# Performance work log

Hardware: AMD Instinct MI355X
Metric: run time of the kernel (lower is better)

The kernel has to match this reference:

```python
import jax, jax.numpy as jnp
import numpy as np

B, S, NX = 2, 2048, 1024
N_STATE, N_HEAD = 1024, 16
HEAD_DIM = N_STATE // N_HEAD


def setup_inputs() -> dict:
    key = jax.random.key(0)
    k1, k2, k3 = jax.random.split(key, 3)
    x = jax.random.normal(k1, (B, S, NX), dtype=jnp.float32)
    w_c = jax.random.normal(k2, (NX, 3 * N_STATE), dtype=jnp.float32) * 0.02
    b_c = jnp.zeros((3 * N_STATE,), dtype=jnp.float32)
    w_p = jax.random.normal(k3, (NX, N_STATE), dtype=jnp.float32) * 0.02
    b_p = jnp.zeros((N_STATE,), dtype=jnp.float32)
    return {"x": x, "w_c": w_c, "b_c": b_c, "w_p": w_p, "b_p": b_p}


def reference(x, w_c, b_c, w_p, b_p):
    # c_attn: 1x1 conv == dense over last dim -> [B, S, 3*n_state]
    c = jnp.einsum('bsn,nf->bsf', x, w_c) + b_c
    q, k, v = jnp.split(c, 3, axis=2)

    def split_heads(t):  # [B,S,n_state] -> [B,H,S,D]
        return t.reshape(B, S, N_HEAD, HEAD_DIM).transpose(0, 2, 1, 3)

    q = split_heads(q)
    k = split_heads(k)  # we contract over D directly instead of transposing to [B,H,D,S]
    v = split_heads(v)

    # scores [B,H,S,S], scaled by rsqrt(head_dim) (scale=True)
    w = jnp.einsum('bhqd,bhkd->bhqk', q, k) * jax.lax.rsqrt(jnp.float32(HEAD_DIM))
    # band mask exactly as in source: w*b + -1e9*(1-b)
    band = jnp.tril(jnp.ones((S, S), dtype=jnp.float32))[None, None]
    w = w * band + (-1e9) * (1.0 - band)
    w = jax.nn.softmax(w, axis=-1)
    a = jnp.einsum('bhqk,bhkd->bhqd', w, v)

    # merge heads -> [B,S,n_state]
    a = a.transpose(0, 2, 1, 3).reshape(B, S, N_STATE)
    # c_proj
    out = jnp.einsum('bsn,nf->bsf', a, w_p) + b_p
    return out
```

## Files before the change

### kernel.cpp

```cpp
#include <hip/hip_runtime.h>
#include <math.h>

#define BATCH 2
#define SEQ 2048
#define NX 1024
#define NSTATE 1024
#define NHEAD 16
#define HDIM 64
#define QKV_LD (3*NSTATE)

typedef __attribute__((ext_vector_type(4))) float f32x4;
typedef __attribute__((ext_vector_type(8))) short bf16x8;

__device__ __forceinline__ unsigned short f2bf(float x) {
    unsigned int u = __float_as_uint(x);
    u = (u + 0x7FFFu + ((u >> 16) & 1u)) >> 16;
    return (unsigned short)u;
}

__device__ __forceinline__ unsigned int cvtpk_bf16(float a, float b) {
    unsigned int r;
    asm("v_cvt_pk_bf16_f32 %0, %1, %2" : "=v"(r) : "v"(a), "v"(b));
    return r;
}

#define GLL(src, dst) __builtin_amdgcn_global_load_lds( \
    (const __attribute__((address_space(1))) void*)(src), \
    (__attribute__((address_space(3))) void*)(dst), 16, 0, 0)

__global__ __launch_bounds__(256) void prep_kernel(
    const float* __restrict__ x, const float* __restrict__ w_c,
    const float* __restrict__ w_p,
    unsigned short* __restrict__ xbf, unsigned short* __restrict__ wcT,
    unsigned short* __restrict__ wpT)
{
    const int bx = blockIdx.x;
    const int t = threadIdx.x;
    if (bx < 4096) {
        int i = bx * 256 + t;
        float4 v = ((const float4*)x)[i];
        ushort4 o;
        o.x = f2bf(v.x); o.y = f2bf(v.y); o.z = f2bf(v.z); o.w = f2bf(v.w);
        ((ushort4*)xbf)[i] = o;
        return;
    }
    __shared__ float tile[64][65];
    const float* in;
    unsigned short* out;
    int R, C, c0, r0;
    if (bx < 4096 + 768) {
        int idx = bx - 4096;
        in = w_c; out = wcT; R = NX; C = 3 * NSTATE;
        c0 = (idx % 48) * 64; r0 = (idx / 48) * 64;
    } else {
        int idx = bx - 4864;
        in = w_p; out = wpT; R = NX; C = NSTATE;
        c0 = (idx % 16) * 64; r0 = (idx / 16) * 64;
    }
    const int cc = t & 63;
    const int rb = t >> 6;
    #pragma unroll
    for (int i = 0; i < 16; i++) {
        int rr = rb + i * 4;
        tile[rr][cc] = in[(size_t)(r0 + rr) * C + c0 + cc];
    }
    __syncthreads();
    #pragma unroll
    for (int i = 0; i < 16; i++) {
        int rr = rb + i * 4;
        out[(size_t)(c0 + rr) * R + r0 + cc] = f2bf(tile[cc][rr]);
    }
}

__global__ __launch_bounds__(256) void vtrans_kernel(
    const unsigned short* __restrict__ qkv, unsigned short* __restrict__ vt)
{
    __shared__ unsigned short t[64][72];
    const int s0 = blockIdx.x * 64;
    const int bh = blockIdx.y;
    const int b = bh >> 4, h = bh & 15;
    const int r = threadIdx.x >> 2;
    const int cg = (threadIdx.x & 3) * 16;
    const unsigned short* src = qkv + (size_t)(b * SEQ + s0 + r) * QKV_LD
                                + 2 * NSTATE + h * HDIM + cg;
    *(bf16x8*)&t[r][cg]     = *(const bf16x8*)src;
    *(bf16x8*)&t[r][cg + 8] = *(const bf16x8*)(src + 8);
    __syncthreads();
    unsigned short tmp[16];
    #pragma unroll
    for (int i = 0; i < 16; i++) tmp[i] = t[cg + i][r];
    unsigned short* dst = vt + (size_t)(bh * 64 + r) * SEQ + s0 + cg;
    *(bf16x8*)dst       = ((const bf16x8*)tmp)[0];
    *(bf16x8*)(dst + 8) = ((const bf16x8*)tmp)[1];
}

template<int RX, int RY, int NBX, bool BF16_OUT>
__global__ __launch_bounds__(256) void gemm_bf16(
    const unsigned short* __restrict__ A,
    const unsigned short* __restrict__ BT,
    const float* __restrict__ bias,
    void* __restrict__ Cv, int M, int N, int K)
{
    const int flat = blockIdx.x;
    const int xcd = flat & 7;
    const int j = flat >> 3;
    const int bx = (xcd % (NBX / RX)) * RX + (j % RX);
    const int by = (xcd / (NBX / RX)) * RY + (j / RX);

    __shared__ unsigned short Als[128 * 32];
    __shared__ unsigned short Bls[128 * 32];
    const int tid = threadIdx.x;
    const int wave = tid >> 6, lane = tid & 63;
    const int bm = bx * 128, bn = by * 128;
    const int wr = (wave >> 1) * 64, wc = (wave & 1) * 64;

    f32x4 acc[4][4];
    #pragma unroll
    for (int m = 0; m < 4; m++)
        #pragma unroll
        for (int n = 0; n < 4; n++)
            acc[m][n] = (f32x4){0.f, 0.f, 0.f, 0.f};

    const int arow = tid >> 2;
    const int ac8 = (tid & 3) * 8;
    char* alds0 = (char*)Als + wave * 1024;
    char* blds0 = (char*)Bls + wave * 1024;
    const int fr = lane & 15, kq = (lane >> 4) * 8;

    for (int k0 = 0; k0 < K; k0 += 32) {
        const unsigned short* ga0 = A  + (size_t)(bm + arow) * K + k0 + ac8;
        const unsigned short* gb0 = BT + (size_t)(bn + arow) * K + k0 + ac8;
        GLL(ga0, alds0);
        GLL(ga0 + (size_t)64 * K, alds0 + 4096);
        GLL(gb0, blds0);
        GLL(gb0 + (size_t)64 * K, blds0 + 4096);
        __syncthreads();

        bf16x8 af[4], bfr[4];
        #pragma unroll
        for (int m = 0; m < 4; m++)
            af[m] = *(const bf16x8*)&Als[(wr + m * 16 + fr) * 32 + kq];
        #pragma unroll
        for (int n = 0; n < 4; n++)
            bfr[n] = *(const bf16x8*)&Bls[(wc + n * 16 + fr) * 32 + kq];
        #pragma unroll
        for (int m = 0; m < 4; m++)
            #pragma unroll
            for (int n = 0; n < 4; n++)
                acc[m][n] = __builtin_amdgcn_mfma_f32_16x16x32_bf16(
                    af[m], bfr[n], acc[m][n], 0, 0, 0);
        __syncthreads();
    }

    const int cr = (lane >> 4) * 4;
    const int ccol = lane & 15;
    #pragma unroll
    for (int m = 0; m < 4; m++) {
        const int row = bm + wr + m * 16 + cr;
        #pragma unroll
        for (int n = 0; n < 4; n++) {
            const int col = bn + wc + n * 16 + ccol;
            const float bv = bias[col];
            #pragma unroll
            for (int j2 = 0; j2 < 4; j2++) {
                float v = acc[m][n][j2] + bv;
                if (BF16_OUT)
                    ((unsigned short*)Cv)[(size_t)(row + j2) * N + col] = f2bf(v);
                else
                    ((float*)Cv)[(size_t)(row + j2) * N + col] = v;
            }
        }
    }
}

template<int RX, int RY, int NBX, bool BF16_OUT>
__global__ __launch_bounds__(256) void gemm_bf16_s(
    const unsigned short* __restrict__ A,
    const unsigned short* __restrict__ BT,
    const float* __restrict__ bias,
    void* __restrict__ Cv, int M, int N, int K)
{
    const int flat = blockIdx.x;
    const int xcd = flat & 7;
    const int j = flat >> 3;
    const int bx = (xcd % (NBX / RX)) * RX + (j % RX);
    const int by = (xcd / (NBX / RX)) * RY + (j / RX);

    __shared__ unsigned short Als[64 * 32];
    __shared__ unsigned short Bls[64 * 32];
    const int tid = threadIdx.x;
    const int wave = tid >> 6, lane = tid & 63;
    const int bm = bx * 64, bn = by * 64;
    const int wr = (wave >> 1) * 32, wc = (wave & 1) * 32;

    f32x4 acc[2][2];
    #pragma unroll
    for (int m = 0; m < 2; m++)
        #pragma unroll
        for (int n = 0; n < 2; n++)
            acc[m][n] = (f32x4){0.f, 0.f, 0.f, 0.f};

    const int arow = tid >> 2;
    const int ac8 = (tid & 3) * 8;
    char* alds = (char*)Als + tid * 16;
    char* blds = (char*)Bls + tid * 16;
    const int fr = lane & 15, kq = (lane >> 4) * 8;

    for (int k0 = 0; k0 < K; k0 += 32) {
        GLL(A  + (size_t)(bm + arow) * K + k0 + ac8, alds);
        GLL(BT + (size_t)(bn + arow) * K + k0 + ac8, blds);
        __syncthreads();

        bf16x8 af[2], bfr[2];
        #pragma unroll
        for (int m = 0; m < 2; m++)
            af[m] = *(const bf16x8*)&Als[(wr + m * 16 + fr) * 32 + kq];
        #pragma unroll
        for (int n = 0; n < 2; n++)
            bfr[n] = *(const bf16x8*)&Bls[(wc + n * 16 + fr) * 32 + kq];
        #pragma unroll
        for (int m = 0; m < 2; m++)
            #pragma unroll
            for (int n = 0; n < 2; n++)
                acc[m][n] = __builtin_amdgcn_mfma_f32_16x16x32_bf16(
                    af[m], bfr[n], acc[m][n], 0, 0, 0);
        __syncthreads();
    }

    const int cr = (lane >> 4) * 4;
    const int ccol = lane & 15;
    #pragma unroll
    for (int m = 0; m < 2; m++) {
        const int row = bm + wr + m * 16 + cr;
        #pragma unroll
        for (int n = 0; n < 2; n++) {
            const int col = bn + wc + n * 16 + ccol;
            const float bv = bias[col];
            #pragma unroll
            for (int j2 = 0; j2 < 4; j2++) {
                float v = acc[m][n][j2] + bv;
                if (BF16_OUT)
                    ((unsigned short*)Cv)[(size_t)(row + j2) * N + col] = f2bf(v);
                else
                    ((float*)Cv)[(size_t)(row + j2) * N + col] = v;
            }
        }
    }
}

__global__ __launch_bounds__(256) void attn_mfma(
    const unsigned short* __restrict__ qkv,
    const unsigned short* __restrict__ vt,
    unsigned short* __restrict__ a_out)
{
    const int f = blockIdx.x;
    const int k_ = f >> 8;
    const int u = (f >> 5) & 7;
    const int bh = f & 31;
    const int qb = (k_ & 1) ? (k_ * 8 + 7 - u) : (k_ * 8 + u);
    const int b = bh >> 4, h = bh & 15;
    const int tid = threadIdx.x;
    const int w = tid >> 6, lane = tid & 63;
    const int c = lane & 15, hh = lane >> 4;

    __shared__ unsigned short Kls[2 * 64 * 64];
    __shared__ unsigned short Vls[2 * 64 * 64];
    __shared__ unsigned short Pls[4][16 * 64];

    const float Cc = 0.18033688f;

    const int o0 = tid * 16;
    const int r0 = o0 >> 7, sc0 = (o0 & 127) ^ ((r0 & 7) << 4);
    const int o1 = 4096 + tid * 16;
    const int r1 = o1 >> 7, sc1 = (o1 & 127) ^ ((r1 & 7) << 4);

    char* kld = (char*)Kls + w * 1024;
    char* vld = (char*)Vls + w * 1024;
    const char* gkbase = (const char*)(qkv + (size_t)b * SEQ * QKV_LD + NSTATE + h * HDIM);
    const char* gvbase = (const char*)(vt + (size_t)(b * NHEAD + h) * HDIM * SEQ);

    #define STAGE(kt_, buf_) do { \
        const char* gk = gkbase + (size_t)(kt_) * 64 * 6144; \
        const char* gv = gvbase + (size_t)(kt_) * 128; \
        char* kd = kld + (buf_) * 8192; \
        char* vd = vld + (buf_) * 8192; \
        GLL(gk + (size_t)r0 * 6144 + sc0, kd); \
        GLL(gk + (size_t)r1 * 6144 + sc1, kd + 4096); \
        GLL(gv + (size_t)r0 * 4096 + sc0, vd); \
        GLL(gv + (size_t)r1 * 4096 + sc1, vd + 4096); \
    } while (0)

    const size_t qrow = (size_t)(b * SEQ + qb * 64 + w * 16 + c);
    const unsigned short* qp = qkv + qrow * QKV_LD + h * HDIM;
    bf16x8 qf0 = *(const bf16x8*)(qp + hh * 8);
    bf16x8 qf1 = *(const bf16x8*)(qp + 32 + hh * 8);

    f32x4 acc_o[4];
    #pragma unroll
    for (int n = 0; n < 4; n++) acc_o[n] = (f32x4){0.f, 0.f, 0.f, 0.f};
    float m_run = -1e30f, l = 0.f;

    const int nkt = qb + 1;
    STAGE(0, 0);
    __syncthreads();

    for (int kt = 0; kt < nkt; kt++) {
        const int cur = kt & 1;
        if (kt + 1 < nkt) STAGE(kt + 1, cur ^ 1);

        const char* kb = (const char*)Kls + cur * 8192;
        const char* vb = (const char*)Vls + cur * 8192;

        f32x4 sacc[4];
        __builtin_amdgcn_s_setprio(1);
        #pragma unroll
        for (int m = 0; m < 4; m++) {
            const int row = m * 16 + c;
            const int sw = (row & 7) << 4;
            bf16x8 kf0 = *(const bf16x8*)(kb + row * 128 + ((hh * 16) ^ sw));
            bf16x8 kf1 = *(const bf16x8*)(kb + row * 128 + ((64 + hh * 16) ^ sw));
            f32x4 z = (f32x4){0.f, 0.f, 0.f, 0.f};
            z = __builtin_amdgcn_mfma_f32_16x16x32_bf16(kf0, qf0, z, 0, 0, 0);
            sacc[m] = __builtin_amdgcn_mfma_f32_16x16x32_bf16(kf1, qf1, z, 0, 0, 0);
        }
        __builtin_amdgcn_s_setprio(0);

        const bool diag = (kt == qb);
        float s[16];
        #pragma unroll
        for (int m = 0; m < 4; m++)
            #pragma unroll
            for (int j = 0; j < 4; j++) {
                float sv = sacc[m][j];
                if (diag) {
                    int klocal = m * 16 + hh * 4 + j;
                    if (klocal > w * 16 + c) sv = -1e30f;
                }
                s[m * 4 + j] = sv;
            }
        float x0 = fmaxf(s[0], s[1]),  x1 = fmaxf(s[2], s[3]);
        float x2 = fmaxf(s[4], s[5]),  x3 = fmaxf(s[6], s[7]);
        float x4 = fmaxf(s[8], s[9]),  x5 = fmaxf(s[10], s[11]);
        float x6 = fmaxf(s[12], s[13]), x7 = fmaxf(s[14], s[15]);
        float y0 = fmaxf(x0, x1), y1 = fmaxf(x2, x3);
        float y2 = fmaxf(x4, x5), y3 = fmaxf(x6, x7);
        float pmax = fmaxf(fmaxf(y0, y1), fmaxf(y2, y3));
        pmax = fmaxf(pmax, __shfl_xor(pmax, 16));
        pmax = fmaxf(pmax, __shfl_xor(pmax, 32));

        if (!__all(pmax <= m_run + 64.0f)) {
            const float mnew = fmaxf(m_run, pmax);
            const float alpha = exp2f((m_run - mnew) * Cc);
            m_run = mnew;
            l *= alpha;
            const float a0 = __shfl(alpha, hh * 4 + 0);
            const float a1 = __shfl(alpha, hh * 4 + 1);
            const float a2 = __shfl(alpha, hh * 4 + 2);
            const float a3 = __shfl(alpha, hh * 4 + 3);
            #pragma unroll
            for (int n = 0; n < 4; n++) {
                acc_o[n][0] *= a0; acc_o[n][1] *= a1;
                acc_o[n][2] *= a2; acc_o[n][3] *= a3;
            }
        }
        const float mc = m_run * Cc;
        float p[16];
        #pragma unroll
        for (int i = 0; i < 16; i++)
            p[i] = exp2f(fmaf(s[i], Cc, -mc));
        {
            float a0 = p[0] + p[1],  a1 = p[2] + p[3];
            float a2 = p[4] + p[5],  a3 = p[6] + p[7];
            float a4 = p[8] + p[9],  a5 = p[10] + p[11];
            float a6 = p[12] + p[13], a7 = p[14] + p[15];
            float b0 = a0 + a1, b1 = a2 + a3, b2 = a4 + a5, b3 = a6 + a7;
            l += (b0 + b1) + (b2 + b3);
        }

        {
            char* pb = (char*)&Pls[w][0] + c * 128;
            const int swp = (c & 7) << 4;
            #pragma unroll
            for (int m = 0; m < 4; m++) {
                uint2 u2;
                u2.x = cvtpk_bf16(p[m * 4 + 0], p[m * 4 + 1]);
                u2.y = cvtpk_bf16(p[m * 4 + 2], p[m * 4 + 3]);
                *(uint2*)(pb + ((m * 32 + hh * 8) ^ swp)) = u2;
            }
        }

        {
            const char* pb = (const char*)&Pls[w][0] + c * 128;
            const int swp = (c & 7) << 4;
            bf16x8 pf0 = *(const bf16x8*)(pb + ((hh * 16) ^ swp));
            bf16x8 pf1 = *(const bf16x8*)(pb + ((64 + hh * 16) ^ swp));
            __builtin_amdgcn_s_setprio(1);
            #pragma unroll
            for (int n = 0; n < 4; n++) {
                const int row = n * 16 + c;
                const int sw = (row & 7) << 4;
                bf16x8 vf0 = *(const bf16x8*)(vb + row * 128 + ((hh * 16) ^ sw));
                bf16x8 vf1 = *(const bf16x8*)(vb + row * 128 + ((64 + hh * 16) ^ sw));
                acc_o[n] = __builtin_amdgcn_mfma_f32_16x16x32_bf16(pf0, vf0, acc_o[n], 0, 0, 0);
                acc_o[n] = __builtin_amdgcn_mfma_f32_16x16x32_bf16(pf1, vf1, acc_o[n], 0, 0, 0);
            }
            __builtin_amdgcn_s_setprio(0);
        }
        __syncthreads();
    }
    #undef STAGE

    l += __shfl_xor(l, 16);
    l += __shfl_xor(l, 32);
    const float linv = 1.f / l;
    const float li0 = __shfl(linv, hh * 4 + 0);
    const float li1 = __shfl(linv, hh * 4 + 1);
    const float li2 = __shfl(linv, hh * 4 + 2);
    const float li3 = __shfl(linv, hh * 4 + 3);
    const size_t orow0 = (size_t)(b * SEQ + qb * 64 + w * 16 + hh * 4);
    #pragma unroll
    for (int n = 0; n < 4; n++) {
        const int col = h * HDIM + n * 16 + c;
        a_out[(orow0 + 0) * NSTATE + col] = f2bf(acc_o[n][0] * li0);
        a_out[(orow0 + 1) * NSTATE + col] = f2bf(acc_o[n][1] * li1);
        a_out[(orow0 + 2) * NSTATE + col] = f2bf(acc_o[n][2] * li2);
        a_out[(orow0 + 3) * NSTATE + col] = f2bf(acc_o[n][3] * li3);
    }
}

extern "C" void kernel_launch(void* const* d_in, const int* in_sizes, int n_in,
                              void* d_out, int out_size, void* d_ws, size_t ws_size,
                              hipStream_t stream)
{
    const float* x   = (const float*)d_in[0];
    const float* w_c = (const float*)d_in[1];
    const float* b_c = (const float*)d_in[2];
    const float* w_p = (const float*)d_in[3];
    const float* b_p = (const float*)d_in[4];
    float* out = (float*)d_out;

    const int M = BATCH * SEQ;

    char* ws = (char*)d_ws;
    unsigned short* qkvbf = (unsigned short*)ws;
    unsigned short* vt    = (unsigned short*)(ws + 25165824);
    unsigned short* xbf   = (unsigned short*)(ws + 25165824 + 8388608);
    unsigned short* wcT   = (unsigned short*)(ws + 25165824 + 2*8388608);
    unsigned short* wpT   = (unsigned short*)(ws + 25165824 + 2*8388608 + 6291456);

    prep_kernel<<<5120, 256, 0, stream>>>(x, w_c, w_p, xbf, wcT, wpT);

    gemm_bf16<8, 12, 32, true><<<768, 256, 0, stream>>>(
        xbf, wcT, b_c, qkvbf, M, 3 * NSTATE, NX);

    vtrans_kernel<<<dim3(SEQ / 64, BATCH * NHEAD), 256, 0, stream>>>(qkvbf, vt);

    attn_mfma<<<1024, 256, 0, stream>>>(qkvbf, vt, xbf);

    gemm_bf16_s<16, 8, 64, false><<<1024, 256, 0, stream>>>(
        xbf, wpT, b_p, out, M, NSTATE, NX);
}
```

Measured before the change: 196.6 us.

## Fuse V transpose into QKV GEMM epilogue and pair causal query blocks

The QKV GEMM epilogue now writes the V third of its output directly in transposed [b,h,d,s] layout, which removes the separate vtrans kernel launch and its extra read and write of V. The attention kernel now handles two query blocks per workgroup (qb and 31-qb), sharing the K/V tile loads between them so every workgroup does the same amount of causal work. The grid shrinks from 1024 to 512 workgroups, with more registers per thread and lower occupancy. The V transpose stores are scattered 8-byte writes.

```diff
diff --git a/kernel.cpp b/kernel.cpp
--- a/kernel.cpp
+++ b/kernel.cpp
@@ -72,34 +72,13 @@
     }
 }
 
-__global__ __launch_bounds__(256) void vtrans_kernel(
-    const unsigned short* __restrict__ qkv, unsigned short* __restrict__ vt)
-{
-    __shared__ unsigned short t[64][72];
-    const int s0 = blockIdx.x * 64;
-    const int bh = blockIdx.y;
-    const int b = bh >> 4, h = bh & 15;
-    const int r = threadIdx.x >> 2;
-    const int cg = (threadIdx.x & 3) * 16;
-    const unsigned short* src = qkv + (size_t)(b * SEQ + s0 + r) * QKV_LD
-                                + 2 * NSTATE + h * HDIM + cg;
-    *(bf16x8*)&t[r][cg]     = *(const bf16x8*)src;
-    *(bf16x8*)&t[r][cg + 8] = *(const bf16x8*)(src + 8);
-    __syncthreads();
-    unsigned short tmp[16];
-    #pragma unroll
-    for (int i = 0; i < 16; i++) tmp[i] = t[cg + i][r];
-    unsigned short* dst = vt + (size_t)(bh * 64 + r) * SEQ + s0 + cg;
-    *(bf16x8*)dst       = ((const bf16x8*)tmp)[0];
-    *(bf16x8*)(dst + 8) = ((const bf16x8*)tmp)[1];
-}
-
-template<int RX, int RY, int NBX, bool BF16_OUT>
+template<int RX, int RY, int NBX, bool BF16_OUT, bool WVT>
 __global__ __launch_bounds__(256) void gemm_bf16(
     const unsigned short* __restrict__ A,
     const unsigned short* __restrict__ BT,
     const float* __restrict__ bias,
-    void* __restrict__ Cv, int M, int N, int K)
+    void* __restrict__ Cv, unsigned short* __restrict__ vtout,
+    int M, int N, int K)
 {
     const int flat = blockIdx.x;
     const int xcd = flat & 7;
@@ -154,6 +133,28 @@
 
     const int cr = (lane >> 4) * 4;
     const int ccol = lane & 15;
+    if (WVT && bn >= 2 * NSTATE) {
+        #pragma unroll
+        for (int m = 0; m < 4; m++) {
+            const int row0 = bm + wr + m * 16 + cr;
+            const int bb = row0 >> 11;
+            const int sl = row0 & 2047;
+            #pragma unroll
+            for (int n = 0; n < 4; n++) {
+                const int col = bn + wc + n * 16 + ccol;
+                const float bv = bias[col];
+                const int vcol = col - 2 * NSTATE;
+                unsigned short o4[4];
+                #pragma unroll
+                for (int j2 = 0; j2 < 4; j2++)
+                    o4[j2] = f2bf(acc[m][n][j2] + bv);
+                unsigned short* dst = vtout +
+                    ((size_t)(bb * 16 + (vcol >> 6)) * 64 + (vcol & 63)) * SEQ + sl;
+                *(uint2*)dst = *(const uint2*)o4;
+            }
+        }
+        return;
+    }
     #pragma unroll
     for (int m = 0; m < 4; m++) {
         const int row = bm + wr + m * 16 + cr;
@@ -253,12 +254,9 @@
     const unsigned short* __restrict__ vt,
     unsigned short* __restrict__ a_out)
 {
-    const int f = blockIdx.x;
-    const int k_ = f >> 8;
-    const int u = (f >> 5) & 7;
-    const int bh = f & 31;
-    const int qb = (k_ & 1) ? (k_ * 8 + 7 - u) : (k_ * 8 + u);
-    const int b = bh >> 4, h = bh & 15;
+    const int bx = blockIdx.x;
+    const int qbA = 31 - bx, qbB = bx;
+    const int h = blockIdx.y, b = blockIdx.z;
     const int tid = threadIdx.x;
     const int w = tid >> 6, lane = tid & 63;
     const int c = lane & 15, hh = lane >> 4;
@@ -290,17 +288,22 @@
         GLL(gv + (size_t)r1 * 4096 + sc1, vd + 4096); \
     } while (0)
 
-    const size_t qrow = (size_t)(b * SEQ + qb * 64 + w * 16 + c);
-    const unsigned short* qp = qkv + qrow * QKV_LD + h * HDIM;
-    bf16x8 qf0 = *(const bf16x8*)(qp + hh * 8);
-    bf16x8 qf1 = *(const bf16x8*)(qp + 32 + hh * 8);
-
-    f32x4 acc_o[4];
-    #pragma unroll
-    for (int n = 0; n < 4; n++) acc_o[n] = (f32x4){0.f, 0.f, 0.f, 0.f};
-    float m_run = -1e30f, l = 0.f;
-
-    const int nkt = qb + 1;
+    const unsigned short* qpA = qkv + (size_t)(b * SEQ + qbA * 64 + w * 16 + c) * QKV_LD + h * HDIM;
+    bf16x8 qfA0 = *(const bf16x8*)(qpA + hh * 8);
+    bf16x8 qfA1 = *(const bf16x8*)(qpA + 32 + hh * 8);
+    const unsigned short* qpB = qkv + (size_t)(b * SEQ + qbB * 64 + w * 16 + c) * QKV_LD + h * HDIM;
+    bf16x8 qfB0 = *(const bf16x8*)(qpB + hh * 8);
+    bf16x8 qfB1 = *(const bf16x8*)(qpB + 32 + hh * 8);
+
+    f32x4 accA[4], accB[4];
+    #pragma unroll
+    for (int n = 0; n < 4; n++) {
+        accA[n] = (f32x4){0.f, 0.f, 0.f, 0.f};
+        accB[n] = (f32x4){0.f, 0.f, 0.f, 0.f};
+    }
+    float mA = -1e30f, lA = 0.f, mB = -1e30f, lB = 0.f;
+
+    const int nkt = qbA + 1;
     STAGE(0, 0);
     __syncthreads();
 
@@ -310,8 +313,9 @@
 
         const char* kb = (const char*)Kls + cur * 8192;
         const char* vb = (const char*)Vls + cur * 8192;
-
-        f32x4 sacc[4];
+        const bool doB = (kt <= qbB);
+
+        f32x4 saccA[4], saccB[4];
         __builtin_amdgcn_s_setprio(1);
         #pragma unroll
         for (int m = 0; m < 4; m++) {
@@ -320,64 +324,65 @@
             bf16x8 kf0 = *(const bf16x8*)(kb + row * 128 + ((hh * 16) ^ sw));
             bf16x8 kf1 = *(const bf16x8*)(kb + row * 128 + ((64 + hh * 16) ^ sw));
             f32x4 z = (f32x4){0.f, 0.f, 0.f, 0.f};
-            z = __builtin_amdgcn_mfma_f32_16x16x32_bf16(kf0, qf0, z, 0, 0, 0);
-            sacc[m] = __builtin_amdgcn_mfma_f32_16x16x32_bf16(kf1, qf1, z, 0, 0, 0);
+            z = __builtin_amdgcn_mfma_f32_16x16x32_bf16(kf0, qfA0, z, 0, 0, 0);
+            saccA[m] = __builtin_amdgcn_mfma_f32_16x16x32_bf16(kf1, qfA1, z, 0, 0, 0);
+            if (doB) {
+                f32x4 z2 = (f32x4){0.f, 0.f, 0.f, 0.f};
+                z2 = __builtin_amdgcn_mfma_f32_16x16x32_bf16(kf0, qfB0, z2, 0, 0, 0);
+                saccB[m] = __builtin_amdgcn_mfma_f32_16x16x32_bf16(kf1, qfB1, z2, 0, 0, 0);
+            }
         }
         __builtin_amdgcn_s_setprio(0);
 
-        const bool diag = (kt == qb);
-        float s[16];
-        #pragma unroll
-        for (int m = 0; m < 4; m++)
-            #pragma unroll
-            for (int j = 0; j < 4; j++) {
-                float sv = sacc[m][j];
-                if (diag) {
-                    int klocal = m * 16 + hh * 4 + j;
-                    if (klocal > w * 16 + c) sv = -1e30f;
+        {
+            const bool diag = (kt == qbA);
+            float s[16];
+            #pragma unroll
+            for (int m = 0; m < 4; m++)
+                #pragma unroll
+                for (int j = 0; j < 4; j++) {
+                    float sv = saccA[m][j];
+                    if (diag) {
+                        int klocal = m * 16 + hh * 4 + j;
+                        if (klocal > w * 16 + c) sv = -1e30f;
+                    }
+                    s[m * 4 + j] = sv;
                 }
-                s[m * 4 + j] = sv;
-            }
-        float x0 = fmaxf(s[0], s[1]),  x1 = fmaxf(s[2], s[3]);
-        float x2 = fmaxf(s[4], s[5]),  x3 = fmaxf(s[6], s[7]);
-        float x4 = fmaxf(s[8], s[9]),  x5 = fmaxf(s[10], s[11]);
-        float x6 = fmaxf(s[12], s[13]), x7 = fmaxf(s[14], s[15]);
-        float y0 = fmaxf(x0, x1), y1 = fmaxf(x2, x3);
-        float y2 = fmaxf(x4, x5), y3 = fmaxf(x6, x7);
-        float pmax = fmaxf(fmaxf(y0, y1), fmaxf(y2, y3));
-        pmax = fmaxf(pmax, __shfl_xor(pmax, 16));
-        pmax = fmaxf(pmax, __shfl_xor(pmax, 32));
-
-        if (!__all(pmax <= m_run + 64.0f)) {
-            const float mnew = fmaxf(m_run, pmax);
-            const float alpha = exp2f((m_run - mnew) * Cc);
-            m_run = mnew;
-            l *= alpha;
-            const float a0 = __shfl(alpha, hh * 4 + 0);
-            const float a1 = __shfl(alpha, hh * 4 + 1);
-            const float a2 = __shfl(alpha, hh * 4 + 2);
-            const float a3 = __shfl(alpha, hh * 4 + 3);
-            #pragma unroll
-            for (int n = 0; n < 4; n++) {
-                acc_o[n][0] *= a0; acc_o[n][1] *= a1;
-                acc_o[n][2] *= a2; acc_o[n][3] *= a3;
-            }
-        }
-        const float mc = m_run * Cc;
-        float p[16];
-        #pragma unroll
-        for (int i = 0; i < 16; i++)
-            p[i] = exp2f(fmaf(s[i], Cc, -mc));
-        {
-            float a0 = p[0] + p[1],  a1 = p[2] + p[3];
-            float a2 = p[4] + p[5],  a3 = p[6] + p[7];
-            float a4 = p[8] + p[9],  a5 = p[10] + p[11];
-            float a6 = p[12] + p[13], a7 = p[14] + p[15];
-            float b0 = a0 + a1, b1 = a2 + a3, b2 = a4 + a5, b3 = a6 + a7;
-            l += (b0 + b1) + (b2 + b3);
-        }
-
-        {
+            float x0 = fmaxf(s[0], s[1]),  x1 = fmaxf(s[2], s[3]);
+            float x2 = fmaxf(s[4], s[5]),  x3 = fmaxf(s[6], s[7]);
+            float x4 = fmaxf(s[8], s[9]),  x5 = fmaxf(s[10], s[11]);
+            float x6 = fmaxf(s[12], s[13]), x7 = fmaxf(s[14], s[15]);
+            float pmax = fmaxf(fmaxf(fmaxf(x0, x1), fmaxf(x2, x3)),
+                               fmaxf(fmaxf(x4, x5), fmaxf(x6, x7)));
+            pmax = fmaxf(pmax, __shfl_xor(pmax, 16));
+            pmax = fmaxf(pmax, __shfl_xor(pmax, 32));
+            if (!__all(pmax <= mA + 64.0f)) {
+                const float mnew = fmaxf(mA, pmax);
+                const float alpha = exp2f((mA - mnew) * Cc);
+                mA = mnew;
+                lA *= alpha;
+                const float a0 = __shfl(alpha, hh * 4 + 0);
+                const float a1 = __shfl(alpha, hh * 4 + 1);
+                const float a2 = __shfl(alpha, hh * 4 + 2);
+                const float a3 = __shfl(alpha, hh * 4 + 3);
+                #pragma unroll
+                for (int n = 0; n < 4; n++) {
+                    accA[n][0] *= a0; accA[n][1] *= a1;
+                    accA[n][2] *= a2; accA[n][3] *= a3;
+                }
+            }
+            const float mc = mA * Cc;
+            float p[16];
+            #pragma unroll
+            for (int i = 0; i < 16; i++)
+                p[i] = exp2f(fmaf(s[i], Cc, -mc));
+            {
+                float a0 = p[0] + p[1],  a1 = p[2] + p[3];
+                float a2 = p[4] + p[5],  a3 = p[6] + p[7];
+                float a4 = p[8] + p[9],  a5 = p[10] + p[11];
+                float a6 = p[12] + p[13], a7 = p[14] + p[15];
+                lA += ((a0 + a1) + (a2 + a3)) + ((a4 + a5) + (a6 + a7));
+            }
             char* pb = (char*)&Pls[w][0] + c * 128;
             const int swp = (c & 7) << 4;
             #pragma unroll
@@ -387,11 +392,6 @@
                 u2.y = cvtpk_bf16(p[m * 4 + 2], p[m * 4 + 3]);
                 *(uint2*)(pb + ((m * 32 + hh * 8) ^ swp)) = u2;
             }
-        }
-
-        {
-            const char* pb = (const char*)&Pls[w][0] + c * 128;
-            const int swp = (c & 7) << 4;
             bf16x8 pf0 = *(const bf16x8*)(pb + ((hh * 16) ^ swp));
             bf16x8 pf1 = *(const bf16x8*)(pb + ((64 + hh * 16) ^ swp));
             __builtin_amdgcn_s_setprio(1);
@@ -401,30 +401,109 @@
                 const int sw = (row & 7) << 4;
                 bf16x8 vf0 = *(const bf16x8*)(vb + row * 128 + ((hh * 16) ^ sw));
                 bf16x8 vf1 = *(const bf16x8*)(vb + row * 128 + ((64 + hh * 16) ^ sw));
-                acc_o[n] = __builtin_amdgcn_mfma_f32_16x16x32_bf16(pf0, vf0, acc_o[n], 0, 0, 0);
-                acc_o[n] = __builtin_amdgcn_mfma_f32_16x16x32_bf16(pf1, vf1, acc_o[n], 0, 0, 0);
+                accA[n] = __builtin_amdgcn_mfma_f32_16x16x32_bf16(pf0, vf0, accA[n], 0, 0, 0);
+                accA[n] = __builtin_amdgcn_mfma_f32_16x16x32_bf16(pf1, vf1, accA[n], 0, 0, 0);
             }
             __builtin_amdgcn_s_setprio(0);
         }
+
+        if (doB) {
+            const bool diag = (kt == qbB);
+            float s[16];
+            #pragma unroll
+            for (int m = 0; m < 4; m++)
+                #pragma unroll
+                for (int j = 0; j < 4; j++) {
+                    float sv = saccB[m][j];
+                    if (diag) {
+                        int klocal = m * 16 + hh * 4 + j;
+                        if (klocal > w * 16 + c) sv = -1e30f;
+                    }
+                    s[m * 4 + j] = sv;
+                }
+            float x0 = fmaxf(s[0], s[1]),  x1 = fmaxf(s[2], s[3]);
+            float x2 = fmaxf(s[4], s[5]),  x3 = fmaxf(s[6], s[7]);
+            float x4 = fmaxf(s[8], s[9]),  x5 = fmaxf(s[10], s[11]);
+            float x6 = fmaxf(s[12], s[13]), x7 = fmaxf(s[14], s[15]);
+            float pmax = fmaxf(fmaxf(fmaxf(x0, x1), fmaxf(x2, x3)),
+                               fmaxf(fmaxf(x4, x5), fmaxf(x6, x7)));
+            pmax = fmaxf(pmax, __shfl_xor(pmax, 16));
+            pmax = fmaxf(pmax, __shfl_xor(pmax, 32));
+            if (!__all(pmax <= mB + 64.0f)) {
+                const float mnew = fmaxf(mB, pmax);
+                const float alpha = exp2f((mB - mnew) * Cc);
+                mB = mnew;
+                lB *= alpha;
+                const float a0 = __shfl(alpha, hh * 4 + 0);
+                const float a1 = __shfl(alpha, hh * 4 + 1);
+                const float a2 = __shfl(alpha, hh * 4 + 2);
+                const float a3 = __shfl(alpha, hh * 4 + 3);
+                #pragma unroll
+                for (int n = 0; n < 4; n++) {
+                    accB[n][0] *= a0; accB[n][1] *= a1;
+                    accB[n][2] *= a2; accB[n][3] *= a3;
+                }
+            }
+            const float mc = mB * Cc;
+            float p[16];
+            #pragma unroll
+            for (int i = 0; i < 16; i++)
+                p[i] = exp2f(fmaf(s[i], Cc, -mc));
+            {
+                float a0 = p[0] + p[1],  a1 = p[2] + p[3];
+                float a2 = p[4] + p[5],  a3 = p[6] + p[7];
+                float a4 = p[8] + p[9],  a5 = p[10] + p[11];
+                float a6 = p[12] + p[13], a7 = p[14] + p[15];
+                lB += ((a0 + a1) + (a2 + a3)) + ((a4 + a5) + (a6 + a7));
+            }
+            char* pb = (char*)&Pls[w][0] + c * 128;
+            const int swp = (c & 7) << 4;
+            #pragma unroll
+            for (int m = 0; m < 4; m++) {
+                uint2 u2;
+                u2.x = cvtpk_bf16(p[m * 4 + 0], p[m * 4 + 1]);
+                u2.y = cvtpk_bf16(p[m * 4 + 2], p[m * 4 + 3]);
+                *(uint2*)(pb + ((m * 32 + hh * 8) ^ swp)) = u2;
+            }
+            bf16x8 pf0 = *(const bf16x8*)(pb + ((hh * 16) ^ swp));
+            bf16x8 pf1 = *(const bf16x8*)(pb + ((64 + hh * 16) ^ swp));
+            __builtin_amdgcn_s_setprio(1);
+            #pragma unroll
+            for (int n = 0; n < 4; n++) {
+                const int row = n * 16 + c;
+                const int sw = (row & 7) << 4;
+                bf16x8 vf0 = *(const bf16x8*)(vb + row * 128 + ((hh * 16) ^ sw));
+                bf16x8 vf1 = *(const bf16x8*)(vb + row * 128 + ((64 + hh * 16) ^ sw));
+                accB[n] = __builtin_amdgcn_mfma_f32_16x16x32_bf16(pf0, vf0, accB[n], 0, 0, 0);
+                accB[n] = __builtin_amdgcn_mfma_f32_16x16x32_bf16(pf1, vf1, accB[n], 0, 0, 0);
+            }
+            __builtin_amdgcn_s_setprio(0);
+        }
         __syncthreads();
     }
     #undef STAGE
 
-    l += __shfl_xor(l, 16);
-    l += __shfl_xor(l, 32);
-    const float linv = 1.f / l;
-    const float li0 = __shfl(linv, hh * 4 + 0);
-    const float li1 = __shfl(linv, hh * 4 + 1);
-    const float li2 = __shfl(linv, hh * 4 + 2);
-    const float li3 = __shfl(linv, hh * 4 + 3);
-    const size_t orow0 = (size_t)(b * SEQ + qb * 64 + w * 16 + hh * 4);
-    #pragma unroll
-    for (int n = 0; n < 4; n++) {
-        const int col = h * HDIM + n * 16 + c;
-        a_out[(orow0 + 0) * NSTATE + col] = f2bf(acc_o[n][0] * li0);
-        a_out[(orow0 + 1) * NSTATE + col] = f2bf(acc_o[n][1] * li1);
-        a_out[(orow0 + 2) * NSTATE + col] = f2bf(acc_o[n][2] * li2);
-        a_out[(orow0 + 3) * NSTATE + col] = f2bf(acc_o[n][3] * li3);
+    #pragma unroll
+    for (int gsel = 0; gsel < 2; gsel++) {
+        const int qb = gsel ? qbB : qbA;
+        f32x4* acc = gsel ? accB : accA;
+        float l = gsel ? lB : lA;
+        l += __shfl_xor(l, 16);
+        l += __shfl_xor(l, 32);
+        const float linv = 1.f / l;
+        const float li0 = __shfl(linv, hh * 4 + 0);
+        const float li1 = __shfl(linv, hh * 4 + 1);
+        const float li2 = __shfl(linv, hh * 4 + 2);
+        const float li3 = __shfl(linv, hh * 4 + 3);
+        const size_t orow0 = (size_t)(b * SEQ + qb * 64 + w * 16 + hh * 4);
+        #pragma unroll
+        for (int n = 0; n < 4; n++) {
+            const int col = h * HDIM + n * 16 + c;
+            a_out[(orow0 + 0) * NSTATE + col] = f2bf(acc[n][0] * li0);
+            a_out[(orow0 + 1) * NSTATE + col] = f2bf(acc[n][1] * li1);
+            a_out[(orow0 + 2) * NSTATE + col] = f2bf(acc[n][2] * li2);
+            a_out[(orow0 + 3) * NSTATE + col] = f2bf(acc[n][3] * li3);
+        }
     }
 }
 
@@ -450,12 +529,10 @@
 
     prep_kernel<<<5120, 256, 0, stream>>>(x, w_c, w_p, xbf, wcT, wpT);
 
-    gemm_bf16<8, 12, 32, true><<<768, 256, 0, stream>>>(
-        xbf, wcT, b_c, qkvbf, M, 3 * NSTATE, NX);
-
-    vtrans_kernel<<<dim3(SEQ / 64, BATCH * NHEAD), 256, 0, stream>>>(qkvbf, vt);
-
-    attn_mfma<<<1024, 256, 0, stream>>>(qkvbf, vt, xbf);
+    gemm_bf16<8, 12, 32, true, true><<<768, 256, 0, stream>>>(
+        xbf, wcT, b_c, qkvbf, vt, M, 3 * NSTATE, NX);
+
+    attn_mfma<<<dim3(16, NHEAD, BATCH), 256, 0, stream>>>(qkvbf, vt, xbf);
 
     gemm_bf16_s<16, 8, 64, false><<<1024, 256, 0, stream>>>(
         xbf, wpT, b_p, out, M, NSTATE, NX);
```

After: 211.7 us. +7.7%, slower.
